# Kernel tuning notes

Measured on AMD Instinct MI355X. Metric: run time of the kernel, lower is better.

The kernel has to match this reference:

```python
import jax, jax.numpy as jnp
import numpy as np

N_NODES = 50000
N_EDGES = 800000
D = 128


def gcn_conv(x, W, b, src, dst, num_nodes):
    """PyG GCNConv: x @ W, add self-loops, symmetric normalization, scatter-add, + bias."""
    x = x @ W  # [N, out]
    loop = jnp.arange(num_nodes, dtype=src.dtype)
    s = jnp.concatenate([src, loop])  # [E+N]
    d = jnp.concatenate([dst, loop])
    w = jnp.ones(s.shape[0], x.dtype)  # edge_weight=None -> ones (self-loop fill=1)
    deg = jax.ops.segment_sum(w, d, num_segments=num_nodes)  # [N]
    dinv = jnp.where(deg > 0, jax.lax.rsqrt(deg), 0.0)
    norm = dinv[s] * dinv[d]  # [E+N]
    out = jax.ops.segment_sum(x[s] * norm[:, None], d, num_segments=num_nodes)
    return out + b


def setup_inputs() -> dict:
    key = jax.random.key(0)
    ks = jax.random.split(key, 8)
    sc = 1.0 / np.sqrt(D)
    x = jax.random.normal(ks[0], (N_NODES, D), dtype=jnp.float32)
    edge_index = jax.random.randint(ks[1], (2, N_EDGES), 0, N_NODES)
    W1 = jax.random.normal(ks[2], (D, D), dtype=jnp.float32) * sc
    W2 = jax.random.normal(ks[3], (D, D), dtype=jnp.float32) * sc
    W3 = jax.random.normal(ks[4], (D, D), dtype=jnp.float32) * sc
    b1 = jnp.zeros((D,), jnp.float32)
    b2 = jnp.zeros((D,), jnp.float32)
    b3 = jnp.zeros((D,), jnp.float32)
    return {"x": x, "edge_index": edge_index, "W1": W1, "b1": b1,
            "W2": W2, "b2": b2, "W3": W3, "b3": b3}


def reference(x, edge_index, W1, b1, W2, b2, W3, b3):
    src, dst = edge_index[0], edge_index[1]
    n = x.shape[0]
    x = jax.nn.relu(gcn_conv(x, W1, b1, src, dst, n))
    x = jax.nn.relu(gcn_conv(x, W2, b2, src, dst, n))
    return gcn_conv(x, W3, b3, src, dst, n)
```

## Files before the change

### kernel.cpp

```cpp
#include <hip/hip_runtime.h>
#include <hip/hip_fp16.h>
#include <math.h>

#define D 128
#define PADH 136

typedef __attribute__((ext_vector_type(8))) _Float16 half8;
typedef __attribute__((ext_vector_type(4))) float f32x4;


__global__ void prep_kernel(const float* __restrict__ W1, const float* __restrict__ W2,
                            const float* __restrict__ W3, __half* __restrict__ WhT,
                            int* __restrict__ cnt, int N) {
    int i = blockIdx.x * blockDim.x + threadIdx.x;
    if (i < 3 * D * D) {
        int l = i >> 14;
        int j = i & 16383;
        int n = j >> 7, k = j & 127;
        const float* W = (l == 0) ? W1 : (l == 1) ? W2 : W3;
        WhT[(size_t)i] = __float2half(W[(size_t)k * D + n]);
    }
    if (i < N) cnt[i] = 0;
}


__global__ void count_rank_kernel(const int* __restrict__ dst, int* __restrict__ cnt,
                                  int* __restrict__ rank, int E) {
    int e0 = (blockIdx.x * blockDim.x + threadIdx.x) * 8;
    if (e0 + 7 < E) {
        int4 da = *(const int4*)(dst + e0);
        int4 db = *(const int4*)(dst + e0 + 4);
        int4 ra, rb;
        ra.x = atomicAdd(&cnt[da.x], 1);
        ra.y = atomicAdd(&cnt[da.y], 1);
        ra.z = atomicAdd(&cnt[da.z], 1);
        ra.w = atomicAdd(&cnt[da.w], 1);
        rb.x = atomicAdd(&cnt[db.x], 1);
        rb.y = atomicAdd(&cnt[db.y], 1);
        rb.z = atomicAdd(&cnt[db.z], 1);
        rb.w = atomicAdd(&cnt[db.w], 1);
        *(int4*)(rank + e0)     = ra;
        *(int4*)(rank + e0 + 4) = rb;
    } else {
        for (int e = e0; e < E; ++e) rank[e] = atomicAdd(&cnt[dst[e]], 1);
    }
}

__global__ __launch_bounds__(1024) void scan_kernel(const int* __restrict__ cnt,
                                                    int* __restrict__ rowptr,
                                                    float* __restrict__ dinv,
                                                    int N) {
    __shared__ int wsum[16];
    __shared__ int carry_s;
    int tid  = threadIdx.x;
    int lane = tid & 63;
    int wid  = tid >> 6;
    if (tid == 0) carry_s = 0;
    __syncthreads();
    for (int base = 0; base < N; base += 4096) {
        int i = base + tid * 4;
        int4 v = make_int4(0, 0, 0, 0);
        if (i + 3 < N) v = *(const int4*)(cnt + i);
        else {
            if (i + 0 < N) v.x = cnt[i + 0];
            if (i + 1 < N) v.y = cnt[i + 1];
            if (i + 2 < N) v.z = cnt[i + 2];
            if (i + 3 < N) v.w = cnt[i + 3];
        }
        int s0 = v.x, s1 = s0 + v.y, s2 = s1 + v.z, s3 = s2 + v.w;
        int sc = s3;
        #pragma unroll
        for (int off = 1; off < 64; off <<= 1) {
            int t = __shfl_up(sc, off, 64);
            if (lane >= off) sc += t;
        }
        if (lane == 63) wsum[wid] = sc;
        __syncthreads();
        if (tid < 16) {
            int w = wsum[tid];
            #pragma unroll
            for (int off = 1; off < 16; off <<= 1) {
                int t = __shfl_up(w, off, 64);
                if (tid >= off) w += t;
            }
            wsum[tid] = w;
        }
        __syncthreads();
        int waveoff = (wid > 0) ? wsum[wid - 1] : 0;
        int excl = carry_s + waveoff + (sc - s3);
        if (i + 0 < N) { rowptr[i + 0] = excl;      dinv[i + 0] = rsqrtf((float)v.x + 1.0f); }
        if (i + 1 < N) { rowptr[i + 1] = excl + s0; dinv[i + 1] = rsqrtf((float)v.y + 1.0f); }
        if (i + 2 < N) { rowptr[i + 2] = excl + s1; dinv[i + 2] = rsqrtf((float)v.z + 1.0f); }
        if (i + 3 < N) { rowptr[i + 3] = excl + s2; dinv[i + 3] = rsqrtf((float)v.w + 1.0f); }
        __syncthreads();
        if (tid == 0) carry_s += wsum[15];
        __syncthreads();
    }
    if (tid == 0) rowptr[N] = carry_s;
}


#define GATHER(vv, cc) __half2 vv = ((const __half2*)(g + (size_t)(cc) * D))[lane]

__device__ __forceinline__ float2 gather_row(const __half* __restrict__ g,
                                             const int* __restrict__ rowptr,
                                             const int* __restrict__ col,
                                             int row, int lane) {
    int s = rowptr[row], e = rowptr[row + 1];
    __half2 hself = ((const __half2*)(g + (size_t)row * D))[lane];
    float2 a0 = __half22float2(hself);
    float2 a1 = make_float2(0.f, 0.f), a2 = make_float2(0.f, 0.f),
           a3 = make_float2(0.f, 0.f), a4 = make_float2(0.f, 0.f),
           a5 = make_float2(0.f, 0.f), a6 = make_float2(0.f, 0.f),
           a7 = make_float2(0.f, 0.f);

    for (int base = s; base < e; base += 64) {
        int idx = base + lane;
        int myc = (idx < e) ? col[idx] : 0;
        int nb  = min(64, e - base);
        int j = 0;
        for (; j + 16 <= nb; j += 16) {
            int c0 = __shfl(myc, j + 0),  c1 = __shfl(myc, j + 1);
            int c2 = __shfl(myc, j + 2),  c3 = __shfl(myc, j + 3);
            int c4 = __shfl(myc, j + 4),  c5 = __shfl(myc, j + 5);
            int c6 = __shfl(myc, j + 6),  c7 = __shfl(myc, j + 7);
            int c8 = __shfl(myc, j + 8),  c9 = __shfl(myc, j + 9);
            int cA = __shfl(myc, j + 10), cB = __shfl(myc, j + 11);
            int cC = __shfl(myc, j + 12), cD = __shfl(myc, j + 13);
            int cE = __shfl(myc, j + 14), cF = __shfl(myc, j + 15);
            GATHER(v0, c0); GATHER(v1, c1); GATHER(v2, c2); GATHER(v3, c3);
            GATHER(v4, c4); GATHER(v5, c5); GATHER(v6, c6); GATHER(v7, c7);
            GATHER(v8, c8); GATHER(v9, c9); GATHER(vA, cA); GATHER(vB, cB);
            GATHER(vC, cC); GATHER(vD, cD); GATHER(vE, cE); GATHER(vF, cF);
            a0.x += __low2float(v0); a0.y += __high2float(v0);
            a1.x += __low2float(v1); a1.y += __high2float(v1);
            a2.x += __low2float(v2); a2.y += __high2float(v2);
            a3.x += __low2float(v3); a3.y += __high2float(v3);
            a4.x += __low2float(v4); a4.y += __high2float(v4);
            a5.x += __low2float(v5); a5.y += __high2float(v5);
            a6.x += __low2float(v6); a6.y += __high2float(v6);
            a7.x += __low2float(v7); a7.y += __high2float(v7);
            a0.x += __low2float(v8); a0.y += __high2float(v8);
            a1.x += __low2float(v9); a1.y += __high2float(v9);
            a2.x += __low2float(vA); a2.y += __high2float(vA);
            a3.x += __low2float(vB); a3.y += __high2float(vB);
            a4.x += __low2float(vC); a4.y += __high2float(vC);
            a5.x += __low2float(vD); a5.y += __high2float(vD);
            a6.x += __low2float(vE); a6.y += __high2float(vE);
            a7.x += __low2float(vF); a7.y += __high2float(vF);
        }
        for (; j + 8 <= nb; j += 8) {
            int c0 = __shfl(myc, j + 0), c1 = __shfl(myc, j + 1);
            int c2 = __shfl(myc, j + 2), c3 = __shfl(myc, j + 3);
            int c4 = __shfl(myc, j + 4), c5 = __shfl(myc, j + 5);
            int c6 = __shfl(myc, j + 6), c7 = __shfl(myc, j + 7);
            GATHER(v0, c0); GATHER(v1, c1); GATHER(v2, c2); GATHER(v3, c3);
            GATHER(v4, c4); GATHER(v5, c5); GATHER(v6, c6); GATHER(v7, c7);
            a0.x += __low2float(v0); a0.y += __high2float(v0);
            a1.x += __low2float(v1); a1.y += __high2float(v1);
            a2.x += __low2float(v2); a2.y += __high2float(v2);
            a3.x += __low2float(v3); a3.y += __high2float(v3);
            a4.x += __low2float(v4); a4.y += __high2float(v4);
            a5.x += __low2float(v5); a5.y += __high2float(v5);
            a6.x += __low2float(v6); a6.y += __high2float(v6);
            a7.x += __low2float(v7); a7.y += __high2float(v7);
        }
        for (; j + 4 <= nb; j += 4) {
            int c0 = __shfl(myc, j + 0), c1 = __shfl(myc, j + 1);
            int c2 = __shfl(myc, j + 2), c3 = __shfl(myc, j + 3);
            GATHER(v0, c0); GATHER(v1, c1); GATHER(v2, c2); GATHER(v3, c3);
            a0.x += __low2float(v0); a0.y += __high2float(v0);
            a1.x += __low2float(v1); a1.y += __high2float(v1);
            a2.x += __low2float(v2); a2.y += __high2float(v2);
            a3.x += __low2float(v3); a3.y += __high2float(v3);
        }
        for (; j < nb; ++j) {
            int c = __shfl(myc, j);
            GATHER(v, c);
            a0.x += __low2float(v); a0.y += __high2float(v);
        }
    }
    a0.x += a1.x + a2.x + a3.x + a4.x + a5.x + a6.x + a7.x;
    a0.y += a1.y + a2.y + a3.y + a4.y + a5.y + a6.y + a7.y;
    return a0;
}


__global__ __launch_bounds__(256) void fill_gemm1_kernel(
    const int* __restrict__ src, const int* __restrict__ dst,
    const int* __restrict__ rank, const int* __restrict__ rowptr,
    int* __restrict__ col, int E, int fill_blocks,
    const float* __restrict__ X, const __half* __restrict__ WhT,
    const float* __restrict__ dinv, __half* __restrict__ Y, int M) {
    int tid = threadIdx.x;
    if ((int)blockIdx.x < fill_blocks) {
        int e0 = (blockIdx.x * 256 + tid) * 8;
        if (e0 + 7 < E) {
            int4 da = *(const int4*)(dst + e0);
            int4 db = *(const int4*)(dst + e0 + 4);
            int4 ra = *(const int4*)(rank + e0);
            int4 rb = *(const int4*)(rank + e0 + 4);
            int4 sa = *(const int4*)(src + e0);
            int4 sb = *(const int4*)(src + e0 + 4);
            int p0 = rowptr[da.x] + ra.x;
            int p1 = rowptr[da.y] + ra.y;
            int p2 = rowptr[da.z] + ra.z;
            int p3 = rowptr[da.w] + ra.w;
            int p4 = rowptr[db.x] + rb.x;
            int p5 = rowptr[db.y] + rb.y;
            int p6 = rowptr[db.z] + rb.z;
            int p7 = rowptr[db.w] + rb.w;
            col[p0] = sa.x; col[p1] = sa.y; col[p2] = sa.z; col[p3] = sa.w;
            col[p4] = sb.x; col[p5] = sb.y; col[p6] = sb.z; col[p7] = sb.w;
        } else {
            for (int e = e0; e < E; ++e) col[rowptr[dst[e]] + rank[e]] = src[e];
        }
        return;
    }
    int bid  = blockIdx.x - fill_blocks;
    int wave = tid >> 6;
    int lane = tid & 63;
    int quad = lane >> 4;
    int l16  = lane & 15;
    int m0   = bid * 64 + wave * 16;
    if (m0 >= M) return;

    f32x4 acc[8];
    #pragma unroll
    for (int t = 0; t < 8; ++t) acc[t] = (f32x4)0.0f;

    const float* xrow = X + (size_t)(m0 + l16) * D;

    #pragma unroll
    for (int ks = 0; ks < 4; ++ks) {
        int k0 = ks * 32 + quad * 8;
        float4 x0 = *(const float4*)(xrow + k0);
        float4 x1 = *(const float4*)(xrow + k0 + 4);
        half8 a;
        a[0] = (_Float16)x0.x; a[1] = (_Float16)x0.y;
        a[2] = (_Float16)x0.z; a[3] = (_Float16)x0.w;
        a[4] = (_Float16)x1.x; a[5] = (_Float16)x1.y;
        a[6] = (_Float16)x1.z; a[7] = (_Float16)x1.w;
        #pragma unroll
        for (int t = 0; t < 8; ++t) {
            half8 b = *(const half8*)(WhT + (size_t)(t * 16 + l16) * D + k0);
            acc[t] = __builtin_amdgcn_mfma_f32_16x16x32_f16(a, b, acc[t], 0, 0, 0);
        }
    }

    float4 dv = *(const float4*)(dinv + m0 + quad * 4);
    float dvs[4] = {dv.x, dv.y, dv.z, dv.w};
    #pragma unroll
    for (int t = 0; t < 8; ++t) {
        #pragma unroll
        for (int r = 0; r < 4; ++r) {
            int grow = m0 + quad * 4 + r;
            Y[(size_t)grow * D + t * 16 + l16] = __float2half(acc[t][r] * dvs[r]);
        }
    }
}


__global__ __launch_bounds__(256) void agg_gemm_kernel(
    const __half* __restrict__ ysIn, const int* __restrict__ rowptr,
    const int* __restrict__ col, const float* __restrict__ dinv,
    const float* __restrict__ bias, const __half* __restrict__ WhT,
    __half* __restrict__ ysOut, int M) {
    __shared__ __half lds_h[64 * PADH];
    int tid  = threadIdx.x;
    int wave = tid >> 6;
    int lane = tid & 63;
    int rbase = blockIdx.x * 64 + wave * 16;

    float2 bb = ((const float2*)bias)[lane];
    for (int t = 0; t < 16; ++t) {
        int row = rbase + t;
        if (row < M) {
            float2 a = gather_row(ysIn, rowptr, col, row, lane);
            float dv = dinv[row];
            float rx = bb.x + dv * a.x;
            float ry = bb.y + dv * a.y;
            __half2 hv = __floats2half2_rn(fmaxf(rx, 0.f), fmaxf(ry, 0.f));
            ((__half2*)(lds_h + (size_t)(wave * 16 + t) * PADH))[lane] = hv;
        }
    }
    __syncthreads();

    int quad = lane >> 4;
    int l16  = lane & 15;
    int m0   = rbase;
    if (m0 >= M) return;

    f32x4 acc[8];
    #pragma unroll
    for (int t = 0; t < 8; ++t) acc[t] = (f32x4)0.0f;

    const __half* arow = lds_h + (size_t)(wave * 16 + l16) * PADH;

    #pragma unroll
    for (int ks = 0; ks < 4; ++ks) {
        int k0 = ks * 32 + quad * 8;
        half8 a = *(const half8*)(arow + k0);
        #pragma unroll
        for (int t = 0; t < 8; ++t) {
            half8 b = *(const half8*)(WhT + (size_t)(t * 16 + l16) * D + k0);
            acc[t] = __builtin_amdgcn_mfma_f32_16x16x32_f16(a, b, acc[t], 0, 0, 0);
        }
    }

    float4 dv = *(const float4*)(dinv + m0 + quad * 4);
    float dvs[4] = {dv.x, dv.y, dv.z, dv.w};
    #pragma unroll
    for (int t = 0; t < 8; ++t) {
        #pragma unroll
        for (int r = 0; r < 4; ++r) {
            int grow = m0 + quad * 4 + r;
            ysOut[(size_t)grow * D + t * 16 + l16] = __float2half(acc[t][r] * dvs[r]);
        }
    }
}


__global__ __launch_bounds__(256) void agg_final_kernel(
    const __half* __restrict__ ys, const int* __restrict__ rowptr,
    const int* __restrict__ col, const float* __restrict__ dinv,
    const float* __restrict__ b, float* __restrict__ out, int N) {
    int gwave = (blockIdx.x * blockDim.x + threadIdx.x) >> 6;
    int lane  = threadIdx.x & 63;
    if (gwave >= N) return;
    float2 a  = gather_row(ys, rowptr, col, gwave, lane);
    float dv  = dinv[gwave];
    float2 bb = ((const float2*)b)[lane];
    ((float2*)(out + (size_t)gwave * D))[lane] = make_float2(bb.x + dv * a.x, bb.y + dv * a.y);
}


extern "C" void kernel_launch(void* const* d_in, const int* in_sizes, int n_in,
                              void* d_out, int out_size, void* d_ws, size_t ws_size,
                              hipStream_t stream) {
    const float* x   = (const float*)d_in[0];
    const int*   ei  = (const int*)d_in[1];
    const float* W1  = (const float*)d_in[2];
    const float* b1  = (const float*)d_in[3];
    const float* W2  = (const float*)d_in[4];
    const float* b2  = (const float*)d_in[5];
    const float* W3  = (const float*)d_in[6];
    const float* b3  = (const float*)d_in[7];
    float* out = (float*)d_out;

    const int N = in_sizes[0] / D;
    const int E = in_sizes[1] / 2;
    const int* src = ei;
    const int* dst = ei + E;

    char* ws = (char*)d_ws;
    size_t off = 0;
    auto alloc = [&](size_t bytes) {
        void* p = ws + off;
        off = (off + bytes + 255) & ~(size_t)255;
        return p;
    };
    __half* ys    = (__half*)alloc((size_t)N * D * sizeof(__half));
    __half* hs    = (__half*)alloc((size_t)N * D * sizeof(__half));
    int*   cnt    = (int*)alloc((size_t)N * sizeof(int));
    int*   rowptr = (int*)alloc((size_t)(N + 1) * sizeof(int));
    float* dinv   = (float*)alloc((size_t)N * sizeof(float));
    int*   rank   = (int*)alloc((size_t)E * sizeof(int));
    int*   col    = (int*)alloc((size_t)E * sizeof(int));
    __half* WhT   = (__half*)alloc((size_t)3 * D * D * sizeof(__half));
    (void)ws_size; (void)n_in; (void)out_size;

    int prep_threads = (3 * D * D > N) ? 3 * D * D : N;
    prep_kernel<<<(prep_threads + 255) / 256, 256, 0, stream>>>(W1, W2, W3, WhT, cnt, N);

    const int egrid = ((E + 7) / 8 + 255) / 256;
    count_rank_kernel<<<egrid, 256, 0, stream>>>(dst, cnt, rank, E);
    scan_kernel<<<1, 1024, 0, stream>>>(cnt, rowptr, dinv, N);

    const int gemm_grid = (N + 63) / 64;
    fill_gemm1_kernel<<<egrid + gemm_grid, 256, 0, stream>>>(
        src, dst, rank, rowptr, col, E, egrid, x, WhT, dinv, ys, N);

    agg_gemm_kernel<<<gemm_grid, 256, 0, stream>>>(ys, rowptr, col, dinv, b1, WhT + 16384, hs, N);
    agg_gemm_kernel<<<gemm_grid, 256, 0, stream>>>(hs, rowptr, col, dinv, b2, WhT + 32768, ys, N);

    const int agg_grid = (N * 64 + 255) / 256;
    agg_final_kernel<<<agg_grid, 256, 0, stream>>>(ys, rowptr, col, dinv, b3, out, N);
}
```

Before: 332.5 us.

## Use chunked single-pass scan and split agg-gemm tiles across waves

The scan kernel now gives each thread a contiguous chunk, sums it, does one block-wide scan, then writes rowptr and dinv in a second pass. This replaces the loop of about 13 iterations, each with several barriers. The aggregation+GEMM kernel now handles 16 rows per block instead of 64. Each wave gathers 4 rows and computes 2 of the 8 output column tiles, which gives 4x more blocks and shorter per-wave serial gather chains, with more parallelism for the latency-bound gather. The cost is more redundant loads of the weight tiles and more blocks launched.

Measured after the change: 311.4 us. 1.07x faster.

```diff
diff --git a/kernel.cpp b/kernel.cpp
--- a/kernel.cpp
+++ b/kernel.cpp
@@ -51,52 +51,64 @@
                                                     float* __restrict__ dinv,
                                                     int N) {
     __shared__ int wsum[16];
-    __shared__ int carry_s;
     int tid  = threadIdx.x;
     int lane = tid & 63;
     int wid  = tid >> 6;
-    if (tid == 0) carry_s = 0;
+    int C = ((N + 4095) / 4096) * 4;
+    int start = tid * C;
+    int end   = start + C; if (end > N) end = N;
+
+    int local = 0;
+    int i = start;
+    for (; i + 3 < end; i += 4) {
+        int4 v = *(const int4*)(cnt + i);
+        local += v.x + v.y + v.z + v.w;
+    }
+    for (; i < end; ++i) local += cnt[i];
+
+    int sc = local;
+    #pragma unroll
+    for (int off = 1; off < 64; off <<= 1) {
+        int t = __shfl_up(sc, off, 64);
+        if (lane >= off) sc += t;
+    }
+    if (lane == 63) wsum[wid] = sc;
     __syncthreads();
-    for (int base = 0; base < N; base += 4096) {
-        int i = base + tid * 4;
-        int4 v = make_int4(0, 0, 0, 0);
-        if (i + 3 < N) v = *(const int4*)(cnt + i);
-        else {
-            if (i + 0 < N) v.x = cnt[i + 0];
-            if (i + 1 < N) v.y = cnt[i + 1];
-            if (i + 2 < N) v.z = cnt[i + 2];
-            if (i + 3 < N) v.w = cnt[i + 3];
-        }
-        int s0 = v.x, s1 = s0 + v.y, s2 = s1 + v.z, s3 = s2 + v.w;
-        int sc = s3;
+    if (tid < 16) {
+        int w = wsum[tid];
         #pragma unroll
-        for (int off = 1; off < 64; off <<= 1) {
-            int t = __shfl_up(sc, off, 64);
-            if (lane >= off) sc += t;
-        }
-        if (lane == 63) wsum[wid] = sc;
-        __syncthreads();
-        if (tid < 16) {
-            int w = wsum[tid];
-            #pragma unroll
-            for (int off = 1; off < 16; off <<= 1) {
-                int t = __shfl_up(w, off, 64);
-                if (tid >= off) w += t;
-            }
-            wsum[tid] = w;
-        }
-        __syncthreads();
-        int waveoff = (wid > 0) ? wsum[wid - 1] : 0;
-        int excl = carry_s + waveoff + (sc - s3);
-        if (i + 0 < N) { rowptr[i + 0] = excl;      dinv[i + 0] = rsqrtf((float)v.x + 1.0f); }
-        if (i + 1 < N) { rowptr[i + 1] = excl + s0; dinv[i + 1] = rsqrtf((float)v.y + 1.0f); }
-        if (i + 2 < N) { rowptr[i + 2] = excl + s1; dinv[i + 2] = rsqrtf((float)v.z + 1.0f); }
-        if (i + 3 < N) { rowptr[i + 3] = excl + s2; dinv[i + 3] = rsqrtf((float)v.w + 1.0f); }
-        __syncthreads();
-        if (tid == 0) carry_s += wsum[15];
-        __syncthreads();
-    }
-    if (tid == 0) rowptr[N] = carry_s;
+        for (int off = 1; off < 16; off <<= 1) {
+            int t = __shfl_up(w, off, 16);
+            if (tid >= off) w += t;
+        }
+        wsum[tid] = w;
+    }
+    __syncthreads();
+    int run = ((wid > 0) ? wsum[wid - 1] : 0) + (sc - local);
+
+    i = start;
+    for (; i + 3 < end; i += 4) {
+        int4 v = *(const int4*)(cnt + i);
+        int4 rp;
+        rp.x = run;
+        rp.y = rp.x + v.x;
+        rp.z = rp.y + v.y;
+        rp.w = rp.z + v.z;
+        run  = rp.w + v.w;
+        *(int4*)(rowptr + i) = rp;
+        float4 dv;
+        dv.x = rsqrtf((float)v.x + 1.0f);
+        dv.y = rsqrtf((float)v.y + 1.0f);
+        dv.z = rsqrtf((float)v.z + 1.0f);
+        dv.w = rsqrtf((float)v.w + 1.0f);
+        *(float4*)(dinv + i) = dv;
+    }
+    for (; i < end; ++i) {
+        int v = cnt[i];
+        rowptr[i] = run; run += v;
+        dinv[i] = rsqrtf((float)v + 1.0f);
+    }
+    if (tid == 0) rowptr[N] = wsum[15];
 }
 
 
@@ -266,56 +278,52 @@
     const int* __restrict__ col, const float* __restrict__ dinv,
     const float* __restrict__ bias, const __half* __restrict__ WhT,
     __half* __restrict__ ysOut, int M) {
-    __shared__ __half lds_h[64 * PADH];
+    __shared__ __half lds_h[16 * PADH];
     int tid  = threadIdx.x;
     int wave = tid >> 6;
     int lane = tid & 63;
-    int rbase = blockIdx.x * 64 + wave * 16;
+    int rbase = blockIdx.x * 16;
 
     float2 bb = ((const float2*)bias)[lane];
-    for (int t = 0; t < 16; ++t) {
-        int row = rbase + t;
+    #pragma unroll
+    for (int t = 0; t < 4; ++t) {
+        int row = rbase + wave * 4 + t;
         if (row < M) {
             float2 a = gather_row(ysIn, rowptr, col, row, lane);
             float dv = dinv[row];
             float rx = bb.x + dv * a.x;
             float ry = bb.y + dv * a.y;
             __half2 hv = __floats2half2_rn(fmaxf(rx, 0.f), fmaxf(ry, 0.f));
-            ((__half2*)(lds_h + (size_t)(wave * 16 + t) * PADH))[lane] = hv;
+            ((__half2*)(lds_h + (size_t)(wave * 4 + t) * PADH))[lane] = hv;
         }
     }
     __syncthreads();
 
+    if (rbase >= M) return;
     int quad = lane >> 4;
     int l16  = lane & 15;
-    int m0   = rbase;
-    if (m0 >= M) return;
-
-    f32x4 acc[8];
-    #pragma unroll
-    for (int t = 0; t < 8; ++t) acc[t] = (f32x4)0.0f;
-
-    const __half* arow = lds_h + (size_t)(wave * 16 + l16) * PADH;
+    int t0   = wave * 2;
+
+    f32x4 acc0 = (f32x4)0.0f, acc1 = (f32x4)0.0f;
+    const __half* arow = lds_h + (size_t)l16 * PADH;
 
     #pragma unroll
     for (int ks = 0; ks < 4; ++ks) {
         int k0 = ks * 32 + quad * 8;
-        half8 a = *(const half8*)(arow + k0);
-        #pragma unroll
-        for (int t = 0; t < 8; ++t) {
-            half8 b = *(const half8*)(WhT + (size_t)(t * 16 + l16) * D + k0);
-            acc[t] = __builtin_amdgcn_mfma_f32_16x16x32_f16(a, b, acc[t], 0, 0, 0);
-        }
-    }
-
-    float4 dv = *(const float4*)(dinv + m0 + quad * 4);
-    float dvs[4] = {dv.x, dv.y, dv.z, dv.w};
-    #pragma unroll
-    for (int t = 0; t < 8; ++t) {
-        #pragma unroll
-        for (int r = 0; r < 4; ++r) {
-            int grow = m0 + quad * 4 + r;
-            ysOut[(size_t)grow * D + t * 16 + l16] = __float2half(acc[t][r] * dvs[r]);
+        half8 a  = *(const half8*)(arow + k0);
+        half8 b0 = *(const half8*)(WhT + (size_t)((t0 + 0) * 16 + l16) * D + k0);
+        half8 b1 = *(const half8*)(WhT + (size_t)((t0 + 1) * 16 + l16) * D + k0);
+        acc0 = __builtin_amdgcn_mfma_f32_16x16x32_f16(a, b0, acc0, 0, 0, 0);
+        acc1 = __builtin_amdgcn_mfma_f32_16x16x32_f16(a, b1, acc1, 0, 0, 0);
+    }
+
+    #pragma unroll
+    for (int r = 0; r < 4; ++r) {
+        int grow = rbase + quad * 4 + r;
+        if (grow < M) {
+            float dvr = dinv[grow];
+            ysOut[(size_t)grow * D + (t0 + 0) * 16 + l16] = __float2half(acc0[r] * dvr);
+            ysOut[(size_t)grow * D + (t0 + 1) * 16 + l16] = __float2half(acc1[r] * dvr);
         }
     }
 }
@@ -377,12 +385,13 @@
     count_rank_kernel<<<egrid, 256, 0, stream>>>(dst, cnt, rank, E);
     scan_kernel<<<1, 1024, 0, stream>>>(cnt, rowptr, dinv, N);
 
-    const int gemm_grid = (N + 63) / 64;
-    fill_gemm1_kernel<<<egrid + gemm_grid, 256, 0, stream>>>(
+    const int gemm1_grid = (N + 63) / 64;
+    fill_gemm1_kernel<<<egrid + gemm1_grid, 256, 0, stream>>>(
         src, dst, rank, rowptr, col, E, egrid, x, WhT, dinv, ys, N);
 
-    agg_gemm_kernel<<<gemm_grid, 256, 0, stream>>>(ys, rowptr, col, dinv, b1, WhT + 16384, hs, N);
-    agg_gemm_kernel<<<gemm_grid, 256, 0, stream>>>(hs, rowptr, col, dinv, b2, WhT + 32768, ys, N);
+    const int agg_gemm_grid = (N + 15) / 16;
+    agg_gemm_kernel<<<agg_gemm_grid, 256, 0, stream>>>(ys, rowptr, col, dinv, b1, WhT + 16384, hs, N);
+    agg_gemm_kernel<<<agg_gemm_grid, 256, 0, stream>>>(hs, rowptr, col, dinv, b2, WhT + 32768, ys, N);
 
     const int agg_grid = (N * 64 + 255) / 256;
     agg_final_kernel<<<agg_grid, 256, 0, stream>>>(ys, rowptr, col, dinv, b3, out, N);
```
